# Kernel tuning notes

Measured on AMD Instinct MI355X. Metric: run time of the kernel, lower is better.

Reference implementation:

```python
import jax, jax.numpy as jnp
import numpy as np

TEMPERATURE = 0.1

def _l2norm(x):
    # F.normalize(dim=1) with eps clamp
    n = jnp.maximum(jnp.linalg.norm(x, axis=1, keepdims=True), 1e-12)
    return x / n

def _retrieval_metric(s):
    # T=1: position of the diagonal element in each row's descending sort.
    order = jnp.argsort(-s, axis=1)            # [N,N] descending argsort
    rankpos = jnp.argsort(order, axis=1)        # inverse permutation: rank of each column
    pos = jnp.diagonal(rankpos)                 # j such that rank[i][j] == i
    posf = pos.astype(s.dtype)
    r1 = jnp.mean((pos < 1).astype(s.dtype))
    r5 = jnp.mean((pos < 5).astype(s.dtype))
    r10 = jnp.mean((pos < 10).astype(s.dtype))
    mr = jnp.mean(posf)
    return r1, r5, r10, mr

def setup_inputs() -> dict:
    key = jax.random.key(0)
    k1, k2, k3, k4 = jax.random.split(key, 4)
    N, C = 4096, 512
    return {
        'v_feat': jax.random.normal(k1, (N, C), dtype=jnp.float32),
        't_feat': jax.random.normal(k2, (N, C), dtype=jnp.float32),
        'p_v': jax.random.normal(k3, (N, C), dtype=jnp.float32),
        'p_t': jax.random.normal(k4, (N, C), dtype=jnp.float32),
    }

def reference(v_feat, t_feat, p_v, p_t):
    vn = _l2norm(v_feat)
    tn = _l2norm(t_feat)
    pvn = _l2norm(p_v)
    ptn = _l2norm(p_t)
    sv = jnp.einsum('nc,mc->nm', vn, ptn) / TEMPERATURE  # [N,N]
    st = jnp.einsum('nc,mc->nm', tn, pvn) / TEMPERATURE  # [N,N]
    # nominator: scalar logsumexp over both diagonals (2N values)
    nominator = jax.nn.logsumexp(jnp.concatenate([jnp.diagonal(sv), jnp.diagonal(st)], axis=0))
    # denominator: per-row logsumexp over concatenated [N,2N]
    denominator = jax.nn.logsumexp(jnp.concatenate([sv, st], axis=1), axis=1)
    loss = jnp.mean(denominator - nominator)
    # metrics (no-grad path in original)
    v_std = jnp.mean(jnp.std(vn, axis=0, ddof=1))
    t_std = jnp.mean(jnp.std(tn, axis=0, ddof=1))
    pv_std = jnp.mean(jnp.std(pvn, axis=0, ddof=1))
    pt_std = jnp.mean(jnp.std(ptn, axis=0, ddof=1))
    sv_raw = jnp.einsum('nc,mc->nm', vn, ptn)
    st_raw = jnp.einsum('nc,mc->nm', tn, pvn)
    v_r1, v_r5, v_r10, v_mr = _retrieval_metric(sv_raw)
    t_r1, t_r5, t_r10, t_mr = _retrieval_metric(st_raw)
    return (loss, v_std, t_std, pv_std, pt_std,
            v_r1, v_r5, v_r10, v_mr,
            t_r1, t_r5, t_r10, t_mr)
```

## Files before the change

kernel.cpp:

```cpp
#include <hip/hip_runtime.h>
#include <hip/hip_bf16.h>

#define N 4096
#define C 512

typedef __attribute__((ext_vector_type(8))) short bf16x8;
typedef __attribute__((ext_vector_type(8))) short s16x8;
typedef __attribute__((ext_vector_type(4))) float f32x4;

__device__ inline float bf2f(__hip_bfloat16 h) { return __bfloat162float(h); }

__device__ inline void gload16(const void* g, void* l) {
    __builtin_amdgcn_global_load_lds(
        (__attribute__((address_space(1))) void*)(g),
        (__attribute__((address_space(3))) void*)(l),
        16, 0, 0);
}

__global__ __launch_bounds__(256) void k_prep(
    const float* __restrict__ s0, const float* __restrict__ s1f,
    const float* __restrict__ s2f, const float* __restrict__ s3,
    __hip_bfloat16* __restrict__ ws_hi0, long mat_stride,
    float* __restrict__ dv, float* __restrict__ dt,
    float* __restrict__ colsum, float* __restrict__ colsq)
{
    __shared__ float sa[4][512];
    __shared__ float sq[4][512];

    const int b = blockIdx.x;
    const int tid = threadIdx.x;
    const int lane = tid & 63;
    const int w = tid >> 6;

    const int pair = b >> 8;
    const int chunk = b & 255;
    const float* X = pair ? s1f : s0;
    const float* B = pair ? s2f : s3;
    const int mX = pair ? 1 : 0;
    const int mB = pair ? 2 : 3;
    __hip_bfloat16* hiX = ws_hi0 + (long)mX * mat_stride;
    __hip_bfloat16* loX = hiX + (long)N * C;
    __hip_bfloat16* hiB = ws_hi0 + (long)mB * mat_stride;
    __hip_bfloat16* loB = hiB + (long)N * C;
    float* dout = pair ? dt : dv;

    float aX[8], qX[8], aB[8], qB[8];
    for (int e = 0; e < 8; e++) { aX[e] = 0.f; qX[e] = 0.f; aB[e] = 0.f; qB[e] = 0.f; }

    const int row0 = chunk * 16 + w * 4;
    for (int i = 0; i < 4; i++) {
        const int row = row0 + i;
        const float4* x4 = (const float4*)(X + (size_t)row * C);
        const float4* b4 = (const float4*)(B + (size_t)row * C);
        float4 x0 = x4[lane * 2], x1 = x4[lane * 2 + 1];
        float4 b0 = b4[lane * 2], b1 = b4[lane * 2 + 1];

        float ss  = x0.x*x0.x + x0.y*x0.y + x0.z*x0.z + x0.w*x0.w
                  + x1.x*x1.x + x1.y*x1.y + x1.z*x1.z + x1.w*x1.w;
        float ssb = b0.x*b0.x + b0.y*b0.y + b0.z*b0.z + b0.w*b0.w
                  + b1.x*b1.x + b1.y*b1.y + b1.z*b1.z + b1.w*b1.w;
        float dot = x0.x*b0.x + x0.y*b0.y + x0.z*b0.z + x0.w*b0.w
                  + x1.x*b1.x + x1.y*b1.y + x1.z*b1.z + x1.w*b1.w;
        for (int o = 1; o < 64; o <<= 1) {
            ss  += __shfl_xor(ss, o);
            ssb += __shfl_xor(ssb, o);
            dot += __shfl_xor(dot, o);
        }
        float scX = 1.0f / fmaxf(sqrtf(ss), 1e-12f);
        float scB = 1.0f / fmaxf(sqrtf(ssb), 1e-12f);
        if (lane == 0) dout[row] = dot * scX * scB;

        float yx[8] = { x0.x*scX, x0.y*scX, x0.z*scX, x0.w*scX,
                        x1.x*scX, x1.y*scX, x1.z*scX, x1.w*scX };
        float yb[8] = { b0.x*scB, b0.y*scB, b0.z*scB, b0.w*scB,
                        b1.x*scB, b1.y*scB, b1.z*scB, b1.w*scB };
        __hip_bfloat16 hvx[8], lvx[8], hvb[8], lvb[8];
        for (int e = 0; e < 8; e++) {
            hvx[e] = __float2bfloat16(yx[e]);
            lvx[e] = __float2bfloat16(yx[e] - bf2f(hvx[e]));
            aX[e] += yx[e]; qX[e] += yx[e] * yx[e];
            hvb[e] = __float2bfloat16(yb[e]);
            lvb[e] = __float2bfloat16(yb[e] - bf2f(hvb[e]));
            aB[e] += yb[e]; qB[e] += yb[e] * yb[e];
        }
        size_t base = (size_t)row * C + lane * 8;
        *(s16x8*)(hiX + base) = *(s16x8*)hvx;
        *(s16x8*)(loX + base) = *(s16x8*)lvx;
        *(s16x8*)(hiB + base) = *(s16x8*)hvb;
        *(s16x8*)(loB + base) = *(s16x8*)lvb;
    }

    for (int e = 0; e < 8; e++) { sa[w][lane*8+e] = aX[e]; sq[w][lane*8+e] = qX[e]; }
    __syncthreads();
    for (int c = tid; c < 512; c += 256) {
        atomicAdd(&colsum[mX * 512 + c], sa[0][c] + sa[1][c] + sa[2][c] + sa[3][c]);
        atomicAdd(&colsq [mX * 512 + c], sq[0][c] + sq[1][c] + sq[2][c] + sq[3][c]);
    }
    __syncthreads();
    for (int e = 0; e < 8; e++) { sa[w][lane*8+e] = aB[e]; sq[w][lane*8+e] = qB[e]; }
    __syncthreads();
    for (int c = tid; c < 512; c += 256) {
        atomicAdd(&colsum[mB * 512 + c], sa[0][c] + sa[1][c] + sa[2][c] + sa[3][c]);
        atomicAdd(&colsq [mB * 512 + c], sq[0][c] + sq[1][c] + sq[2][c] + sq[3][c]);
    }
}

__global__ __launch_bounds__(256) void k_gemm(
    const __hip_bfloat16* __restrict__ h0, const __hip_bfloat16* __restrict__ l0,
    const __hip_bfloat16* __restrict__ h1, const __hip_bfloat16* __restrict__ l1,
    const __hip_bfloat16* __restrict__ h2, const __hip_bfloat16* __restrict__ l2,
    const __hip_bfloat16* __restrict__ h3, const __hip_bfloat16* __restrict__ l3,
    const float* __restrict__ dv, const float* __restrict__ dt,
    float* __restrict__ row_ev, float* __restrict__ row_et,
    float* __restrict__ row_cv, float* __restrict__ row_ct)
{
    __shared__ __align__(16) __hip_bfloat16 sA[2][128][32];
    __shared__ __align__(16) __hip_bfloat16 sB[2][128][32];
    __shared__ float sdiag[128];
    __shared__ float sred[128][2][2];

    const int z = blockIdx.z;
    const __hip_bfloat16* Ah = z ? h1 : h0;
    const __hip_bfloat16* Al = z ? l1 : l0;
    const __hip_bfloat16* Bh = z ? h2 : h3;
    const __hip_bfloat16* Bl = z ? l2 : l3;
    const float* diag = z ? dt : dv;
    float* row_e = z ? row_et : row_ev;
    float* row_c = z ? row_ct : row_cv;

    const int tid = threadIdx.x;
    const int lane = tid & 63;
    const int w = tid >> 6;
    const int wy = w >> 1, wx = w & 1;
    const int bm = blockIdx.x * 128;
    const int bn = blockIdx.y * 128;

    if (tid < 128) sdiag[tid] = diag[bm + tid];

    f32x4 acc[4][4];
    for (int i = 0; i < 4; i++)
        for (int j = 0; j < 4; j++)
            acc[i][j] = (f32x4){0.f, 0.f, 0.f, 0.f};

    const int srow = lane >> 2;
    const int lcol = (lane & 3) * 8;
    const int scolg = (((lane & 3) ^ ((lane >> 3) & 3))) * 8;
    const int fr = lane & 15;
    const int pcs = ((lane >> 4) ^ ((fr >> 1) & 3)) * 8;

    for (int k0 = 0; k0 < C; k0 += 32) {
        for (int half = 0; half < 2; half++) {
            int rr = w * 16 + half * 64 + srow;
            size_t ga = (size_t)(bm + rr) * C + k0 + scolg;
            size_t gb = (size_t)(bn + rr) * C + k0 + scolg;
            gload16(Ah + ga, &sA[0][rr][lcol]);
            gload16(Al + ga, &sA[1][rr][lcol]);
            gload16(Bh + gb, &sB[0][rr][lcol]);
            gload16(Bl + gb, &sB[1][rr][lcol]);
        }
        __syncthreads();

        bf16x8 a_h[4], a_l[4], b_h[4], b_l[4];
        for (int i = 0; i < 4; i++) {
            a_h[i] = *(const bf16x8*)&sA[0][wy * 64 + i * 16 + fr][pcs];
            a_l[i] = *(const bf16x8*)&sA[1][wy * 64 + i * 16 + fr][pcs];
            b_h[i] = *(const bf16x8*)&sB[0][wx * 64 + i * 16 + fr][pcs];
            b_l[i] = *(const bf16x8*)&sB[1][wx * 64 + i * 16 + fr][pcs];
        }
        for (int i = 0; i < 4; i++)
            for (int j = 0; j < 4; j++) {
                acc[i][j] = __builtin_amdgcn_mfma_f32_16x16x32_bf16(a_h[i], b_h[j], acc[i][j], 0, 0, 0);
                acc[i][j] = __builtin_amdgcn_mfma_f32_16x16x32_bf16(a_h[i], b_l[j], acc[i][j], 0, 0, 0);
                acc[i][j] = __builtin_amdgcn_mfma_f32_16x16x32_bf16(a_l[i], b_h[j], acc[i][j], 0, 0, 0);
            }
        __syncthreads();
    }

    const int quad = lane >> 4;
    for (int i = 0; i < 4; i++) {
        for (int reg = 0; reg < 4; reg++) {
            int rloc = wy * 64 + i * 16 + quad * 4 + reg;
            int grow = bm + rloc;
            float d = sdiag[rloc];
            float e = 0.f, c = 0.f;
            for (int j = 0; j < 4; j++) {
                float s = acc[i][j][reg];
                int gcol = bn + wx * 64 + j * 16 + fr;
                e += __expf(10.f * s - 10.f);
                if (s > d && gcol != grow) c += 1.f;
            }
            for (int o = 1; o < 16; o <<= 1) {
                e += __shfl_xor(e, o);
                c += __shfl_xor(c, o);
            }
            if (fr == 0) { sred[rloc][wx][0] = e; sred[rloc][wx][1] = c; }
        }
    }
    __syncthreads();
    if (tid < 128) {
        atomicAdd(&row_e[bm + tid], sred[tid][0][0] + sred[tid][1][0]);
        atomicAdd(&row_c[bm + tid], sred[tid][0][1] + sred[tid][1][1]);
    }
}

__global__ __launch_bounds__(256) void k_fin(
    const float* __restrict__ dv, const float* __restrict__ dt,
    const float* __restrict__ row_ev, const float* __restrict__ row_et,
    const float* __restrict__ row_cv, const float* __restrict__ row_ct,
    const float* __restrict__ colsum, const float* __restrict__ colsq,
    float* __restrict__ out)
{
    const int t = threadIdx.x;
    const int lane = t & 63;
    const int wv = t >> 6;

    float vals[10];
    for (int k = 0; k < 10; k++) vals[k] = 0.f;
    for (int i = 0; i < 16; i++) {
        const int row = i * 256 + t;
        float se = row_ev[row] + row_et[row];
        float pv = row_cv[row];
        float pt = row_ct[row];
        vals[0] += logf(se) + 10.f;
        vals[1] += (pv < 0.5f) ? 1.f : 0.f;
        vals[2] += (pv < 4.5f) ? 1.f : 0.f;
        vals[3] += (pv < 9.5f) ? 1.f : 0.f;
        vals[4] += pv;
        vals[5] += (pt < 0.5f) ? 1.f : 0.f;
        vals[6] += (pt < 4.5f) ? 1.f : 0.f;
        vals[7] += (pt < 9.5f) ? 1.f : 0.f;
        vals[8] += pt;
        vals[9] += __expf(10.f * dv[row] - 10.f) + __expf(10.f * dt[row] - 10.f);
    }
    __shared__ float red[4][10];
    for (int k = 0; k < 10; k++) {
        float v = vals[k];
        for (int o = 1; o < 64; o <<= 1) v += __shfl_xor(v, o);
        if (lane == 0) red[wv][k] = v;
    }

    __shared__ float smat[4][4];
    for (int m = 0; m < 4; m++) {
        float sd2 = 0.f;
        for (int h = 0; h < 2; h++) {
            int c = h * 256 + t;
            float a = colsum[m * 512 + c];
            float q = colsq [m * 512 + c];
            float var = (q - a * a * (1.f / N)) * (1.f / (N - 1));
            sd2 += sqrtf(fmaxf(var, 0.f));
        }
        for (int o = 1; o < 64; o <<= 1) sd2 += __shfl_xor(sd2, o);
        if (lane == 0) smat[wv][m] = sd2;
    }
    __syncthreads();
    if (t == 0) {
        float g[10];
        for (int k = 0; k < 10; k++)
            g[k] = red[0][k] + red[1][k] + red[2][k] + red[3][k];
        float stds[4];
        for (int m = 0; m < 4; m++)
            stds[m] = (smat[0][m] + smat[1][m] + smat[2][m] + smat[3][m]) * (1.f / 512.f);
        const float invN = 1.f / N;
        float nominator = logf(g[9]) + 10.f;
        out[0]  = g[0] * invN - nominator;
        out[1]  = stds[0];
        out[2]  = stds[1];
        out[3]  = stds[2];
        out[4]  = stds[3];
        out[5]  = g[1] * invN;
        out[6]  = g[2] * invN;
        out[7]  = g[3] * invN;
        out[8]  = g[4] * invN;
        out[9]  = g[5] * invN;
        out[10] = g[6] * invN;
        out[11] = g[7] * invN;
        out[12] = g[8] * invN;
    }
}

extern "C" void kernel_launch(void* const* d_in, const int* in_sizes, int n_in,
                              void* d_out, int out_size, void* d_ws, size_t ws_size,
                              hipStream_t stream)
{
    char* p = (char*)d_ws;

    float* row_ev = (float*)p; p += N * 4;
    float* row_et = (float*)p; p += N * 4;
    float* row_cv = (float*)p; p += N * 4;
    float* row_ct = (float*)p; p += N * 4;
    float* colsum = (float*)p; p += 4 * 512 * 4;
    float* colsq  = (float*)p; p += 4 * 512 * 4;
    const size_t acc_bytes = (size_t)(p - (char*)d_ws);

    const size_t NE = (size_t)N * C;
    const long mat_stride = 2 * NE;
    __hip_bfloat16* hiA[4];
    __hip_bfloat16* loA[4];
    for (int m = 0; m < 4; m++) {
        hiA[m] = (__hip_bfloat16*)p; p += NE * 2;
        loA[m] = (__hip_bfloat16*)p; p += NE * 2;
    }
    float* dv = (float*)p; p += N * 4;
    float* dt = (float*)p; p += N * 4;

    hipMemsetAsync(d_ws, 0, acc_bytes, stream);

    k_prep<<<dim3(512), 256, 0, stream>>>(
        (const float*)d_in[0], (const float*)d_in[1],
        (const float*)d_in[2], (const float*)d_in[3],
        hiA[0], mat_stride, dv, dt, colsum, colsq);

    k_gemm<<<dim3(32, 32, 2), 256, 0, stream>>>(
        hiA[0], loA[0], hiA[1], loA[1], hiA[2], loA[2], hiA[3], loA[3],
        dv, dt, row_ev, row_et, row_cv, row_ct);

    k_fin<<<dim3(1), 256, 0, stream>>>(
        dv, dt, row_ev, row_et, row_cv, row_ct, colsum, colsq, (float*)d_out);
}
```

Before: 212.2 us.

## Fuse final reduction into GEMM via last-block counter and overlay shared memory

Removes the separate single-block finalize kernel; each GEMM block bumps a global atomic counter and the last block to finish does the final reductions and writes outputs. Epilogue shared buffers are aliased onto the GEMM tile buffers to cut LDS use, and launch bounds now request 5 waves per SIMD to raise occupancy. This saves one kernel launch and gap. The costs are an extra atomic per block, a serial tail on one block, and possible register pressure or spills from the tighter launch bound.

```diff
diff --git a/kernel.cpp b/kernel.cpp
--- a/kernel.cpp
+++ b/kernel.cpp
@@ -105,19 +105,25 @@
     }
 }
 
-__global__ __launch_bounds__(256) void k_gemm(
+__global__ __launch_bounds__(256, 5) void k_gemm(
     const __hip_bfloat16* __restrict__ h0, const __hip_bfloat16* __restrict__ l0,
     const __hip_bfloat16* __restrict__ h1, const __hip_bfloat16* __restrict__ l1,
     const __hip_bfloat16* __restrict__ h2, const __hip_bfloat16* __restrict__ l2,
     const __hip_bfloat16* __restrict__ h3, const __hip_bfloat16* __restrict__ l3,
     const float* __restrict__ dv, const float* __restrict__ dt,
     float* __restrict__ row_ev, float* __restrict__ row_et,
-    float* __restrict__ row_cv, float* __restrict__ row_ct)
+    float* __restrict__ row_cv, float* __restrict__ row_ct,
+    const float* __restrict__ colsum, const float* __restrict__ colsq,
+    unsigned int* __restrict__ counter, float* __restrict__ out)
 {
     __shared__ __align__(16) __hip_bfloat16 sA[2][128][32];
     __shared__ __align__(16) __hip_bfloat16 sB[2][128][32];
-    __shared__ float sdiag[128];
-    __shared__ float sred[128][2][2];
+    float* ovl   = (float*)&sA[0][0][0];
+    float* sdiag = ovl;
+    float* sred  = ovl + 128;
+    float* fred  = ovl + 640;
+    float* fsmat = ovl + 680;
+    unsigned int* s_old = (unsigned int*)(ovl + 700);
 
     const int z = blockIdx.z;
     const __hip_bfloat16* Ah = z ? h1 : h0;
@@ -134,8 +140,6 @@
     const int wy = w >> 1, wx = w & 1;
     const int bm = blockIdx.x * 128;
     const int bn = blockIdx.y * 128;
-
-    if (tid < 128) sdiag[tid] = diag[bm + tid];
 
     f32x4 acc[4][4];
     for (int i = 0; i < 4; i++)
@@ -175,6 +179,9 @@
             }
         __syncthreads();
     }
+
+    if (tid < 128) sdiag[tid] = diag[bm + tid];
+    __syncthreads();
 
     const int quad = lane >> 4;
     for (int i = 0; i < 4; i++) {
@@ -193,88 +200,86 @@
                 e += __shfl_xor(e, o);
                 c += __shfl_xor(c, o);
             }
-            if (fr == 0) { sred[rloc][wx][0] = e; sred[rloc][wx][1] = c; }
+            if (fr == 0) { sred[(rloc * 2 + wx) * 2 + 0] = e; sred[(rloc * 2 + wx) * 2 + 1] = c; }
         }
     }
     __syncthreads();
     if (tid < 128) {
-        atomicAdd(&row_e[bm + tid], sred[tid][0][0] + sred[tid][1][0]);
-        atomicAdd(&row_c[bm + tid], sred[tid][0][1] + sred[tid][1][1]);
-    }
-}
-
-__global__ __launch_bounds__(256) void k_fin(
-    const float* __restrict__ dv, const float* __restrict__ dt,
-    const float* __restrict__ row_ev, const float* __restrict__ row_et,
-    const float* __restrict__ row_cv, const float* __restrict__ row_ct,
-    const float* __restrict__ colsum, const float* __restrict__ colsq,
-    float* __restrict__ out)
-{
-    const int t = threadIdx.x;
-    const int lane = t & 63;
-    const int wv = t >> 6;
-
-    float vals[10];
-    for (int k = 0; k < 10; k++) vals[k] = 0.f;
-    for (int i = 0; i < 16; i++) {
-        const int row = i * 256 + t;
-        float se = row_ev[row] + row_et[row];
-        float pv = row_cv[row];
-        float pt = row_ct[row];
-        vals[0] += logf(se) + 10.f;
-        vals[1] += (pv < 0.5f) ? 1.f : 0.f;
-        vals[2] += (pv < 4.5f) ? 1.f : 0.f;
-        vals[3] += (pv < 9.5f) ? 1.f : 0.f;
-        vals[4] += pv;
-        vals[5] += (pt < 0.5f) ? 1.f : 0.f;
-        vals[6] += (pt < 4.5f) ? 1.f : 0.f;
-        vals[7] += (pt < 9.5f) ? 1.f : 0.f;
-        vals[8] += pt;
-        vals[9] += __expf(10.f * dv[row] - 10.f) + __expf(10.f * dt[row] - 10.f);
-    }
-    __shared__ float red[4][10];
-    for (int k = 0; k < 10; k++) {
-        float v = vals[k];
-        for (int o = 1; o < 64; o <<= 1) v += __shfl_xor(v, o);
-        if (lane == 0) red[wv][k] = v;
-    }
-
-    __shared__ float smat[4][4];
-    for (int m = 0; m < 4; m++) {
-        float sd2 = 0.f;
-        for (int h = 0; h < 2; h++) {
-            int c = h * 256 + t;
-            float a = colsum[m * 512 + c];
-            float q = colsq [m * 512 + c];
-            float var = (q - a * a * (1.f / N)) * (1.f / (N - 1));
-            sd2 += sqrtf(fmaxf(var, 0.f));
-        }
-        for (int o = 1; o < 64; o <<= 1) sd2 += __shfl_xor(sd2, o);
-        if (lane == 0) smat[wv][m] = sd2;
-    }
-    __syncthreads();
-    if (t == 0) {
-        float g[10];
-        for (int k = 0; k < 10; k++)
-            g[k] = red[0][k] + red[1][k] + red[2][k] + red[3][k];
-        float stds[4];
-        for (int m = 0; m < 4; m++)
-            stds[m] = (smat[0][m] + smat[1][m] + smat[2][m] + smat[3][m]) * (1.f / 512.f);
-        const float invN = 1.f / N;
-        float nominator = logf(g[9]) + 10.f;
-        out[0]  = g[0] * invN - nominator;
-        out[1]  = stds[0];
-        out[2]  = stds[1];
-        out[3]  = stds[2];
-        out[4]  = stds[3];
-        out[5]  = g[1] * invN;
-        out[6]  = g[2] * invN;
-        out[7]  = g[3] * invN;
-        out[8]  = g[4] * invN;
-        out[9]  = g[5] * invN;
-        out[10] = g[6] * invN;
-        out[11] = g[7] * invN;
-        out[12] = g[8] * invN;
+        atomicAdd(&row_e[bm + tid], sred[(tid * 2 + 0) * 2 + 0] + sred[(tid * 2 + 1) * 2 + 0]);
+        atomicAdd(&row_c[bm + tid], sred[(tid * 2 + 0) * 2 + 1] + sred[(tid * 2 + 1) * 2 + 1]);
+    }
+    __syncthreads();
+
+    if (tid == 0) {
+        __threadfence();
+        *s_old = atomicAdd(counter, 1u);
+    }
+    __syncthreads();
+    if (*s_old != 2047) return;
+    __threadfence();
+
+    {
+        const int lane2 = tid & 63;
+        const int wv = tid >> 6;
+        float vals[10];
+        for (int k = 0; k < 10; k++) vals[k] = 0.f;
+        for (int i = 0; i < 16; i++) {
+            const int row = i * 256 + tid;
+            float se = row_ev[row] + row_et[row];
+            float pv = row_cv[row];
+            float pt = row_ct[row];
+            vals[0] += logf(se) + 10.f;
+            vals[1] += (pv < 0.5f) ? 1.f : 0.f;
+            vals[2] += (pv < 4.5f) ? 1.f : 0.f;
+            vals[3] += (pv < 9.5f) ? 1.f : 0.f;
+            vals[4] += pv;
+            vals[5] += (pt < 0.5f) ? 1.f : 0.f;
+            vals[6] += (pt < 4.5f) ? 1.f : 0.f;
+            vals[7] += (pt < 9.5f) ? 1.f : 0.f;
+            vals[8] += pt;
+            vals[9] += __expf(10.f * dv[row] - 10.f) + __expf(10.f * dt[row] - 10.f);
+        }
+        for (int k = 0; k < 10; k++) {
+            float v = vals[k];
+            for (int o = 1; o < 64; o <<= 1) v += __shfl_xor(v, o);
+            if (lane2 == 0) fred[wv * 10 + k] = v;
+        }
+        for (int m = 0; m < 4; m++) {
+            float sd2 = 0.f;
+            for (int h = 0; h < 2; h++) {
+                int c = h * 256 + tid;
+                float a = colsum[m * 512 + c];
+                float q = colsq [m * 512 + c];
+                float var = (q - a * a * (1.f / N)) * (1.f / (N - 1));
+                sd2 += sqrtf(fmaxf(var, 0.f));
+            }
+            for (int o = 1; o < 64; o <<= 1) sd2 += __shfl_xor(sd2, o);
+            if (lane2 == 0) fsmat[wv * 4 + m] = sd2;
+        }
+        __syncthreads();
+        if (tid == 0) {
+            float g[10];
+            for (int k = 0; k < 10; k++)
+                g[k] = fred[0 * 10 + k] + fred[1 * 10 + k] + fred[2 * 10 + k] + fred[3 * 10 + k];
+            float stds[4];
+            for (int m = 0; m < 4; m++)
+                stds[m] = (fsmat[0 * 4 + m] + fsmat[1 * 4 + m] + fsmat[2 * 4 + m] + fsmat[3 * 4 + m]) * (1.f / 512.f);
+            const float invN = 1.f / N;
+            float nominator = logf(g[9]) + 10.f;
+            out[0]  = g[0] * invN - nominator;
+            out[1]  = stds[0];
+            out[2]  = stds[1];
+            out[3]  = stds[2];
+            out[4]  = stds[3];
+            out[5]  = g[1] * invN;
+            out[6]  = g[2] * invN;
+            out[7]  = g[3] * invN;
+            out[8]  = g[4] * invN;
+            out[9]  = g[5] * invN;
+            out[10] = g[6] * invN;
+            out[11] = g[7] * invN;
+            out[12] = g[8] * invN;
+        }
     }
 }
 
@@ -290,6 +295,7 @@
     float* row_ct = (float*)p; p += N * 4;
     float* colsum = (float*)p; p += 4 * 512 * 4;
     float* colsq  = (float*)p; p += 4 * 512 * 4;
+    unsigned int* counter = (unsigned int*)p; p += 16;
     const size_t acc_bytes = (size_t)(p - (char*)d_ws);
 
     const size_t NE = (size_t)N * C;
@@ -312,8 +318,6 @@
 
     k_gemm<<<dim3(32, 32, 2), 256, 0, stream>>>(
         hiA[0], loA[0], hiA[1], loA[1], hiA[2], loA[2], hiA[3], loA[3],
-        dv, dt, row_ev, row_et, row_cv, row_ct);
-
-    k_fin<<<dim3(1), 256, 0, stream>>>(
-        dv, dt, row_ev, row_et, row_cv, row_ct, colsum, colsq, (float*)d_out);
+        dv, dt, row_ev, row_et, row_cv, row_ct,
+        colsum, colsq, counter, (float*)d_out);
 }
```

Result: slower. 844.4 us (+298.0%).
